# Kernel tuning notes

Measured on AMD Instinct MI355X. Metric: run time of the kernel, lower is better.

Reference implementation:

```python
import jax, jax.numpy as jnp
import numpy as np

B, T, I, H = 2048, 4096, 5, 10  # batch, seq_len, input_dim, hidden_dim


def setup_inputs() -> dict:
    key = jax.random.key(0)
    ks = jax.random.split(key, 5)
    return {
        "x": jax.random.normal(ks[0], (B, T, I), dtype=jnp.float32),
        "h0": jnp.zeros((1, B, H), dtype=jnp.float32),
        "c0": jnp.zeros((1, B, H), dtype=jnp.float32),
        "W_ih": jax.random.normal(ks[1], (4 * H, I), dtype=jnp.float32) * 0.3,
        "W_hh": jax.random.normal(ks[2], (4 * H, H), dtype=jnp.float32) * 0.3,
        "b_ih": jax.random.normal(ks[3], (4 * H,), dtype=jnp.float32) * 0.1,
        "b_hh": jax.random.normal(ks[4], (4 * H,), dtype=jnp.float32) * 0.1,
    }


def reference(x, h0, c0, W_ih, W_hh, b_ih, b_hh):
    # Single-layer nn.LSTM (batch_first=True), gate order i,f,g,o.
    # Precompute input contribution for all timesteps: [B,T,4H]
    x_gates = jnp.einsum("bti,gi->btg", x, W_ih) + b_ih + b_hh

    def step(carry, xg_t):
        h, c = carry  # [B,H] each
        gates = xg_t + h @ W_hh.T  # [B,4H]
        i_g, f_g, g_g, o_g = jnp.split(gates, 4, axis=-1)
        i_g = jax.nn.sigmoid(i_g)
        f_g = jax.nn.sigmoid(f_g)
        g_g = jnp.tanh(g_g)
        o_g = jax.nn.sigmoid(o_g)
        c = f_g * c + i_g * g_g
        h = o_g * jnp.tanh(c)
        return (h, c), h

    (_, _), hs = jax.lax.scan(step, (h0[0], c0[0]), jnp.swapaxes(x_gates, 0, 1))
    return jnp.swapaxes(hs, 0, 1)  # [B,T,H], matching lstm_out
```

## Files before the change

### kernel.cpp

```cpp
#include <hip/hip_runtime.h>


#define BB 2048
#define TT 4096
#define II 5
#define HH 10
#define GG 40
#define CH 256
#define CHF (CH * II)
#define NCHUNK (TT / CH)

__device__ __forceinline__ float readlane_f(float v, int l) {
    union { float f; int i; } u;
    u.f = v;
    u.i = __builtin_amdgcn_readlane(u.i, l);
    return u.f;
}

__global__ __launch_bounds__(64) void lstm_wave_kernel(
    const float* __restrict__ x,
    const float* __restrict__ h0,
    const float* __restrict__ c0,
    const float* __restrict__ W_ih,
    const float* __restrict__ W_hh,
    const float* __restrict__ b_ih,
    const float* __restrict__ b_hh,
    float* __restrict__ out)
{
    __shared__ float xs[2][CHF];

    const int b = blockIdx.x;
    const int lane = threadIdx.x;
    const int g = lane;

    float wih[II];
    float whh[HH];
    float bias = 0.f;
    if (g < GG) {
#pragma unroll
        for (int k = 0; k < II; k++) wih[k] = W_ih[g * II + k];
#pragma unroll
        for (int j = 0; j < HH; j++) whh[j] = W_hh[g * HH + j];
        bias = b_ih[g] + b_hh[g];
    } else {
#pragma unroll
        for (int k = 0; k < II; k++) wih[k] = 0.f;
#pragma unroll
        for (int j = 0; j < HH; j++) whh[j] = 0.f;
    }

    const float LOG2E = 1.4426950408889634f;
    const bool is_tanh = (g >= 2 * HH && g < 3 * HH);
    const float k1 = is_tanh ? (-2.f * LOG2E) : (-LOG2E);
    const float am = is_tanh ? 2.f : 1.f;
    const float ac = is_tanh ? -1.f : 0.f;

    float hval = 0.f, cval = 0.f;
    if (lane < HH) {
        hval = h0[b * HH + lane];
        cval = c0[b * HH + lane];
    }

    const float* xrow = x + (size_t)b * TT * II;
    float* orow = out + (size_t)b * TT * HH;

    float4 pf0, pf1, pf2, pf3, pf4;
    {
        const float4* xv = (const float4*)xrow;
        pf0 = xv[0 * 64 + lane];
        pf1 = xv[1 * 64 + lane];
        pf2 = xv[2 * 64 + lane];
        pf3 = xv[3 * 64 + lane];
        pf4 = xv[4 * 64 + lane];
        float4* dst = (float4*)xs[0];
        dst[0 * 64 + lane] = pf0;
        dst[1 * 64 + lane] = pf1;
        dst[2 * 64 + lane] = pf2;
        dst[3 * 64 + lane] = pf3;
        dst[4 * 64 + lane] = pf4;
    }

    for (int c = 0; c < NCHUNK; ++c) {
        const float* xc = xs[c & 1];

        if (c + 1 < NCHUNK) {
            const float4* xv = (const float4*)(xrow + (size_t)(c + 1) * CHF);
            pf0 = xv[0 * 64 + lane];
            pf1 = xv[1 * 64 + lane];
            pf2 = xv[2 * 64 + lane];
            pf3 = xv[3 * 64 + lane];
            pf4 = xv[4 * 64 + lane];
        }

#pragma unroll 8
        for (int u = 0; u < CH; ++u) {
            const int t = c * CH + u;

            const float x0 = xc[u * II + 0];
            const float x1 = xc[u * II + 1];
            const float x2 = xc[u * II + 2];
            const float x3 = xc[u * II + 3];
            const float x4 = xc[u * II + 4];

            float a0 = fmaf(x0, wih[0], bias);
            float a1 = x1 * wih[1];
            float a2 = x2 * wih[2];
            float a3 = x3 * wih[3];
            a0 = fmaf(x4, wih[4], a0);

            a1 = fmaf(readlane_f(hval, 0), whh[0], a1);
            a2 = fmaf(readlane_f(hval, 1), whh[1], a2);
            a3 = fmaf(readlane_f(hval, 2), whh[2], a3);
            a0 = fmaf(readlane_f(hval, 3), whh[3], a0);
            a1 = fmaf(readlane_f(hval, 4), whh[4], a1);
            a2 = fmaf(readlane_f(hval, 5), whh[5], a2);
            a3 = fmaf(readlane_f(hval, 6), whh[6], a3);
            a0 = fmaf(readlane_f(hval, 7), whh[7], a0);
            a1 = fmaf(readlane_f(hval, 8), whh[8], a1);
            a2 = fmaf(readlane_f(hval, 9), whh[9], a2);
            const float acc = (a0 + a1) + (a2 + a3);

            const float e = __builtin_amdgcn_exp2f(acc * k1);
            const float s = __builtin_amdgcn_rcpf(1.f + e);
            const float act = fmaf(s, am, ac);

            const float fv = __shfl(act, lane + HH, 64);
            const float gv = __shfl(act, lane + 2 * HH, 64);
            const float ov = __shfl(act, lane + 3 * HH, 64);

            cval = fmaf(fv, cval, act * gv);
            const float e2 = __builtin_amdgcn_exp2f(cval * (-2.f * LOG2E));
            const float th = fmaf(__builtin_amdgcn_rcpf(1.f + e2), 2.f, -1.f);
            hval = ov * th;

            if (lane < HH) orow[t * HH + lane] = hval;
        }

        if (c + 1 < NCHUNK) {
            float4* dst = (float4*)xs[(c + 1) & 1];
            dst[0 * 64 + lane] = pf0;
            dst[1 * 64 + lane] = pf1;
            dst[2 * 64 + lane] = pf2;
            dst[3 * 64 + lane] = pf3;
            dst[4 * 64 + lane] = pf4;
        }
    }
}

extern "C" void kernel_launch(void* const* d_in, const int* in_sizes, int n_in,
                              void* d_out, int out_size, void* d_ws, size_t ws_size,
                              hipStream_t stream) {
    const float* x    = (const float*)d_in[0];
    const float* h0   = (const float*)d_in[1];
    const float* c0   = (const float*)d_in[2];
    const float* W_ih = (const float*)d_in[3];
    const float* W_hh = (const float*)d_in[4];
    const float* b_ih = (const float*)d_in[5];
    const float* b_hh = (const float*)d_in[6];
    float* out = (float*)d_out;

    lstm_wave_kernel<<<dim3(BB), dim3(64), 0, stream>>>(
        x, h0, c0, W_ih, W_hh, b_ih, b_hh, out);
}
```

Measured before the change: 1.178 ms.

## Interleave LSTM gates per lane quad and broadcast with DPP instead of shuffles

Remaps gate rows so each hidden unit's four gates sit in one quad of adjacent lanes, letting the i/f/g/o exchange use DPP quad broadcasts instead of three ds_bpermute shuffles per step. It also folds the exp2 scaling constants into the weights, bias and cell state, which removes multiplies from the serial recurrence. The trade-off is that the cell state is kept in a scaled domain, which adds rounding risk.

```diff
diff --git a/kernel.cpp b/kernel.cpp
--- a/kernel.cpp
+++ b/kernel.cpp
@@ -5,7 +5,6 @@
 #define TT 4096
 #define II 5
 #define HH 10
-#define GG 40
 #define CH 256
 #define CHF (CH * II)
 #define NCHUNK (TT / CH)
@@ -14,6 +13,14 @@
     union { float f; int i; } u;
     u.f = v;
     u.i = __builtin_amdgcn_readlane(u.i, l);
+    return u.f;
+}
+
+template<int E>
+__device__ __forceinline__ float quad_bcast(float v) {
+    union { float f; int i; } u;
+    u.f = v;
+    u.i = __builtin_amdgcn_update_dpp(u.i, u.i, E * 0x55, 0xF, 0xF, false);
     return u.f;
 }
 
@@ -31,38 +38,43 @@
 
     const int b = blockIdx.x;
     const int lane = threadIdx.x;
-    const int g = lane;
+    const int j = lane >> 2;
+    const int k = lane & 3;
+    const bool active = (lane < 4 * HH);
+
+    const float LOG2E = 1.4426950408889634f;
+    const float KC = -2.f * LOG2E;
+    const float scale = (k == 2) ? KC : -LOG2E;
 
     float wih[II];
     float whh[HH];
     float bias = 0.f;
-    if (g < GG) {
+    if (active) {
+        const int row = k * HH + j;
 #pragma unroll
-        for (int k = 0; k < II; k++) wih[k] = W_ih[g * II + k];
+        for (int q = 0; q < II; q++) wih[q] = W_ih[row * II + q] * scale;
 #pragma unroll
-        for (int j = 0; j < HH; j++) whh[j] = W_hh[g * HH + j];
-        bias = b_ih[g] + b_hh[g];
+        for (int q = 0; q < HH; q++) whh[q] = W_hh[row * HH + q] * scale;
+        bias = (b_ih[row] + b_hh[row]) * scale;
     } else {
 #pragma unroll
-        for (int k = 0; k < II; k++) wih[k] = 0.f;
+        for (int q = 0; q < II; q++) wih[q] = 0.f;
 #pragma unroll
-        for (int j = 0; j < HH; j++) whh[j] = 0.f;
+        for (int q = 0; q < HH; q++) whh[q] = 0.f;
     }
 
-    const float LOG2E = 1.4426950408889634f;
-    const bool is_tanh = (g >= 2 * HH && g < 3 * HH);
-    const float k1 = is_tanh ? (-2.f * LOG2E) : (-LOG2E);
-    const float am = is_tanh ? 2.f : 1.f;
-    const float ac = is_tanh ? -1.f : 0.f;
+    const float am = (k == 2) ? (2.f * KC) : 1.f;
+    const float ac = (k == 2) ? (-KC) : 0.f;
 
-    float hval = 0.f, cval = 0.f;
-    if (lane < HH) {
-        hval = h0[b * HH + lane];
-        cval = c0[b * HH + lane];
+    float hval = 0.f, cs = 0.f;
+    if (active) {
+        hval = h0[b * HH + j];
+        cs   = c0[b * HH + j] * KC;
     }
 
     const float* xrow = x + (size_t)b * TT * II;
     float* orow = out + (size_t)b * TT * HH;
+    const bool do_store = active && (k == 0);
 
     float4 pf0, pf1, pf2, pf3, pf4;
     {
@@ -108,32 +120,33 @@
             float a3 = x3 * wih[3];
             a0 = fmaf(x4, wih[4], a0);
 
-            a1 = fmaf(readlane_f(hval, 0), whh[0], a1);
-            a2 = fmaf(readlane_f(hval, 1), whh[1], a2);
-            a3 = fmaf(readlane_f(hval, 2), whh[2], a3);
-            a0 = fmaf(readlane_f(hval, 3), whh[3], a0);
-            a1 = fmaf(readlane_f(hval, 4), whh[4], a1);
-            a2 = fmaf(readlane_f(hval, 5), whh[5], a2);
-            a3 = fmaf(readlane_f(hval, 6), whh[6], a3);
-            a0 = fmaf(readlane_f(hval, 7), whh[7], a0);
-            a1 = fmaf(readlane_f(hval, 8), whh[8], a1);
-            a2 = fmaf(readlane_f(hval, 9), whh[9], a2);
+            a0 = fmaf(readlane_f(hval, 0),  whh[0], a0);
+            a1 = fmaf(readlane_f(hval, 4),  whh[1], a1);
+            a2 = fmaf(readlane_f(hval, 8),  whh[2], a2);
+            a3 = fmaf(readlane_f(hval, 12), whh[3], a3);
+            a0 = fmaf(readlane_f(hval, 16), whh[4], a0);
+            a1 = fmaf(readlane_f(hval, 20), whh[5], a1);
+            a2 = fmaf(readlane_f(hval, 24), whh[6], a2);
+            a3 = fmaf(readlane_f(hval, 28), whh[7], a3);
+            a0 = fmaf(readlane_f(hval, 32), whh[8], a0);
+            a1 = fmaf(readlane_f(hval, 36), whh[9], a1);
             const float acc = (a0 + a1) + (a2 + a3);
 
-            const float e = __builtin_amdgcn_exp2f(acc * k1);
+            const float e = __builtin_amdgcn_exp2f(acc);
             const float s = __builtin_amdgcn_rcpf(1.f + e);
             const float act = fmaf(s, am, ac);
 
-            const float fv = __shfl(act, lane + HH, 64);
-            const float gv = __shfl(act, lane + 2 * HH, 64);
-            const float ov = __shfl(act, lane + 3 * HH, 64);
+            const float iv = quad_bcast<0>(act);
+            const float fv = quad_bcast<1>(act);
+            const float gs = quad_bcast<2>(act);
+            const float ov = quad_bcast<3>(act);
 
-            cval = fmaf(fv, cval, act * gv);
-            const float e2 = __builtin_amdgcn_exp2f(cval * (-2.f * LOG2E));
+            cs = fmaf(fv, cs, iv * gs);
+            const float e2 = __builtin_amdgcn_exp2f(cs);
             const float th = fmaf(__builtin_amdgcn_rcpf(1.f + e2), 2.f, -1.f);
             hval = ov * th;
 
-            if (lane < HH) orow[t * HH + lane] = hval;
+            if (do_store) orow[t * HH + j] = hval;
         }
 
         if (c + 1 < NCHUNK) {
```

Result: faster. 1.117 ms (-5.2%).
